# Kernel tuning notes

Measured on AMD Instinct MI355X. Metric: run time of the kernel, lower is better.

## Reference

```python
import jax, jax.numpy as jnp
import numpy as np

B, S, E = 4, 4096, 128  # batch, seq_len, embedding_dim (quaternion groups)
D = 4 * E               # flattened feature dim fed to the Linear layers


def setup_inputs() -> dict:
    key = jax.random.key(0)
    ks = jax.random.split(key, 9)
    scale_w = 1.0 / np.sqrt(D).astype(np.float32)
    return {
        "query": jax.random.normal(ks[0], (B, S, E, 4), dtype=jnp.float32),
        "key": jax.random.normal(ks[1], (B, S, E, 4), dtype=jnp.float32),
        "value": jax.random.normal(ks[2], (B, S, E, 4), dtype=jnp.float32),
        "Wq": jax.random.normal(ks[3], (D, D), dtype=jnp.float32) * scale_w,
        "bq": jax.random.normal(ks[4], (D,), dtype=jnp.float32) * 0.01,
        "Wk": jax.random.normal(ks[5], (D, D), dtype=jnp.float32) * scale_w,
        "bk": jax.random.normal(ks[6], (D,), dtype=jnp.float32) * 0.01,
        "Wv": jax.random.normal(ks[7], (D, D), dtype=jnp.float32) * scale_w,
        "bv": jax.random.normal(ks[8], (D,), dtype=jnp.float32) * 0.01,
    }


def reference(query, key, value, Wq, bq, Wk, bk, Wv, bv):
    b, s = query.shape[0], query.shape[1]
    e = query.shape[2]  # embedding_dim
    # flatten quaternion dim: [B,S,E,4] -> [B,S,4E]
    q = query.reshape(b, s, -1)
    k = key.reshape(b, key.shape[1], -1)
    v = value.reshape(b, value.shape[1], -1)
    # torch nn.Linear: x @ W^T + bias
    Q = (q @ Wq.T + bq).reshape(b, s, -1, 4)
    K = (k @ Wk.T + bk).reshape(b, key.shape[1], -1, 4)
    V = (v @ Wv.T + bv).reshape(b, value.shape[1], -1, 4)
    # full QK^T over quaternion-grouped dims: [B,S,S]
    scores = jnp.einsum('bseq,bkeq->bsk', Q, K) / jnp.sqrt(jnp.float32(e))
    weights = jax.nn.softmax(scores, axis=-1)
    # faithful to the source: weights are summed over k and scale V at position s
    output = jnp.einsum('bsk,bseq->bseq', weights, V)
    return output, weights
```

## Files before the change

### kernel.cpp

```cpp
#include <hip/hip_runtime.h>
#include <cstdint>

typedef _Float16 h1;
typedef _Float16 h4 __attribute__((ext_vector_type(4)));
typedef _Float16 h8 __attribute__((ext_vector_type(8)));
typedef float    f4 __attribute__((ext_vector_type(4)));
typedef float    f32x4 __attribute__((ext_vector_type(4)));

#define NB 4
#define SL 4096
#define DD 512
#define MM (NB*SL)
#define SHIFT 12.0f

__global__ __launch_bounds__(256) void convert_all(
    const float* __restrict__ Xq, const float* __restrict__ Xk, const float* __restrict__ Xv,
    const float* __restrict__ Wq, const float* __restrict__ Wk, const float* __restrict__ Wv,
    h1* __restrict__ Xh, h1* __restrict__ Wh)
{
    const int xper = MM*DD/4;
    const int wper = DD*DD/4;
    const int xtot = 3*xper;
    int i = blockIdx.x * 256 + threadIdx.x;
    const float* src;
    h1* dst;
    int j;
    if (i < xtot) {
        int mat = i / xper; j = i - mat*xper;
        src = (mat==0) ? Xq : (mat==1 ? Xk : Xv);
        dst = Xh + (size_t)mat*MM*DD;
    } else {
        int t = i - xtot;
        if (t >= 3*wper) return;
        int mat = t / wper; j = t - mat*wper;
        src = (mat==0) ? Wq : (mat==1 ? Wk : Wv);
        dst = Wh + (size_t)mat*DD*DD;
    }
    f4 v = ((const f4*)src)[j];
    h4 hv;
    hv[0]=(h1)v[0]; hv[1]=(h1)v[1]; hv[2]=(h1)v[2]; hv[3]=(h1)v[3];
    ((h4*)dst)[j] = hv;
}

__device__ __forceinline__ void stage_tile(const h1* __restrict__ gbase,
                                           h1* lds, int w, int l)
{
    #pragma unroll
    for (int j = 0; j < 4; j++) {
        const int cc  = w*4 + j;
        const int row = cc*8 + (l >> 3);
        const int sc  = (l & 7) ^ (l >> 3);
        const h1* src = gbase + (size_t)row * DD + sc*8;
        void* dst = (char*)lds + cc*1024;
        __builtin_amdgcn_global_load_lds(
            (const __attribute__((address_space(1))) uint32_t*)src,
            (__attribute__((address_space(3))) uint32_t*)dst, 16, 0, 0);
    }
}

__device__ __forceinline__ void stage_half(const h1* __restrict__ gbase,
                                           char* ldsbase, int w, int l)
{
    #pragma unroll
    for (int j = 0; j < 2; j++) {
        const int cc  = w*2 + j;
        const int row = cc*8 + (l >> 3);
        const int sc  = (l & 7) ^ (l >> 3);
        const h1* src = gbase + (size_t)row * DD + sc*8;
        __builtin_amdgcn_global_load_lds(
            (const __attribute__((address_space(1))) uint32_t*)src,
            (__attribute__((address_space(3))) uint32_t*)(ldsbase + cc*1024), 16, 0, 0);
    }
}

__device__ __forceinline__ h8 lds_frag(const h1* lds, int row, int lc)
{
    const int chunk = lc ^ (row & 7);
    return *(const h8*)(lds + row*64 + chunk*8);
}

__global__ __launch_bounds__(256) void proj_gemm(
    const h1* __restrict__ Xh, const h1* __restrict__ Wh,
    const float* __restrict__ bq, const float* __restrict__ bk, const float* __restrict__ bv,
    h1* __restrict__ Qh, h1* __restrict__ Kh, float* __restrict__ Vout)
{
    const int prj = blockIdx.z;
    const h1* __restrict__ X    = Xh + (size_t)prj * MM * DD;
    const h1* __restrict__ W    = Wh + (size_t)prj * DD * DD;
    const float* __restrict__ bias = (prj==0) ? bq : (prj==1 ? bk : bv);

    const int m0 = blockIdx.y * 128;
    const int n0 = blockIdx.x * 128;

    __shared__ h1 As[128*64];
    __shared__ h1 Bs[128*64];

    const int tid  = threadIdx.x;
    const int lane = tid & 63;
    const int wid  = tid >> 6;
    const int wm = wid >> 1, wn = wid & 1;
    const int g  = lane >> 4, c = lane & 15;

    f32x4 acc[4][4];
    #pragma unroll
    for (int i = 0; i < 4; i++)
        #pragma unroll
        for (int j = 0; j < 4; j++) acc[i][j] = (f32x4){0.f, 0.f, 0.f, 0.f};

    for (int k0 = 0; k0 < DD; k0 += 64) {
        __syncthreads();
        stage_tile(X + (size_t)m0 * DD + k0, As, wid, lane);
        stage_tile(W + (size_t)n0 * DD + k0, Bs, wid, lane);
        __syncthreads();
        #pragma unroll
        for (int kk = 0; kk < 2; kk++) {
            h8 af[4], bf[4];
            #pragma unroll
            for (int mf = 0; mf < 4; mf++) af[mf] = lds_frag(As, wm*64 + mf*16 + c, kk*4 + g);
            #pragma unroll
            for (int nf = 0; nf < 4; nf++) bf[nf] = lds_frag(Bs, wn*64 + nf*16 + c, kk*4 + g);
            #pragma unroll
            for (int mf = 0; mf < 4; mf++)
                #pragma unroll
                for (int nf = 0; nf < 4; nf++)
                    acc[mf][nf] = __builtin_amdgcn_mfma_f32_16x16x32_f16(af[mf], bf[nf], acc[mf][nf], 0, 0, 0);
        }
    }

    float bv4[4];
    #pragma unroll
    for (int nf = 0; nf < 4; nf++) bv4[nf] = bias[n0 + wn*64 + nf*16 + c];

    #pragma unroll
    for (int mf = 0; mf < 4; mf++) {
        #pragma unroll
        for (int i = 0; i < 4; i++) {
            const int row = m0 + wm*64 + mf*16 + g*4 + i;
            #pragma unroll
            for (int nf = 0; nf < 4; nf++) {
                const int col = n0 + wn*64 + nf*16 + c;
                float vv = acc[mf][nf][i] + bv4[nf];
                if (prj == 0)      Qh[(size_t)row*DD + col] = (h1)vv;
                else if (prj == 1) Kh[(size_t)row*DD + col] = (h1)vv;
                else               Vout[(size_t)row*DD + col] = vv;
            }
        }
    }
}

__global__ __launch_bounds__(512) void scores_gemm_8ph(
    const h1* __restrict__ Qh, const h1* __restrict__ Kh,
    h1* __restrict__ Eh,
    float* __restrict__ partial)
{
    const int orig = blockIdx.x;
    const int swz  = (orig & 7) * 128 + (orig >> 3);
    const int b  = swz >> 8;
    const int t_ = swz & 255;
    const int ty = t_ >> 4;
    const int tx = t_ & 15;
    const int m0 = ty * 256;
    const int n0 = tx * 256;
    const h1* __restrict__ Qb = Qh + (size_t)b * SL * DD;
    const h1* __restrict__ Kb = Kh + (size_t)b * SL * DD;

    __shared__ h1 Albuf[2*256*64];
    __shared__ h1 Blbuf[2*256*64];
    const int SLOT_H = 256*64;
    const int SLOT_B = SLOT_H*2;

    const int tid  = threadIdx.x;
    const int lane = tid & 63;
    const int wid  = tid >> 6;
    const int wm = wid >> 2;
    const int wn = wid & 3;
    const int g  = lane >> 4, c = lane & 15;

    f32x4 acc[8][4];
    #pragma unroll
    for (int i = 0; i < 8; i++)
        #pragma unroll
        for (int j = 0; j < 4; j++) acc[i][j] = (f32x4){0.f, 0.f, 0.f, 0.f};

    stage_half(Qb + (size_t)m0*DD,            (char*)Albuf,          wid, lane);
    stage_half(Qb + (size_t)(m0+128)*DD,      (char*)Albuf + 16384,  wid, lane);
    stage_half(Kb + (size_t)n0*DD,            (char*)Blbuf,          wid, lane);
    stage_half(Kb + (size_t)(n0+128)*DD,      (char*)Blbuf + 16384,  wid, lane);
    asm volatile("s_waitcnt vmcnt(0)" ::: "memory");
    __builtin_amdgcn_s_barrier();

    for (int kt = 0; kt < 8; ++kt) {
        const int cur = kt & 1;
        const h1* Abase = Albuf + cur*SLOT_H;
        const h1* Bbase = Blbuf + cur*SLOT_H;
        #pragma unroll
        for (int q = 0; q < 4; q++) {
            const int mh = q >> 1, nh = q & 1;

            h8 af[4][2], bf[2][2];
            #pragma unroll
            for (int fm = 0; fm < 4; fm++)
                #pragma unroll
                for (int ks = 0; ks < 2; ks++)
                    af[fm][ks] = lds_frag(Abase, wm*128 + (mh*4+fm)*16 + c, ks*4 + g);
            #pragma unroll
            for (int fn = 0; fn < 2; fn++)
                #pragma unroll
                for (int ks = 0; ks < 2; ks++)
                    bf[fn][ks] = lds_frag(Bbase, wn*64 + (nh*2+fn)*16 + c, ks*4 + g);

            if (q == 0 && kt < 7) {
                const int k0n = (kt+1) * 64;
                char* Adst = (char*)Albuf + (cur^1)*SLOT_B;
                char* Bdst = (char*)Blbuf + (cur^1)*SLOT_B;
                stage_half(Qb + (size_t)m0*DD + k0n,       Adst,         wid, lane);
                stage_half(Qb + (size_t)(m0+128)*DD + k0n, Adst + 16384, wid, lane);
                stage_half(Kb + (size_t)n0*DD + k0n,       Bdst,         wid, lane);
                stage_half(Kb + (size_t)(n0+128)*DD + k0n, Bdst + 16384, wid, lane);
            }

            __builtin_amdgcn_s_barrier();
            asm volatile("s_waitcnt lgkmcnt(0)" ::: "memory");
            __builtin_amdgcn_sched_barrier(0);
            __builtin_amdgcn_s_setprio(1);
            #pragma unroll
            for (int fm = 0; fm < 4; fm++)
                #pragma unroll
                for (int fn = 0; fn < 2; fn++)
                    #pragma unroll
                    for (int ks = 0; ks < 2; ks++)
                        acc[mh*4+fm][nh*2+fn] = __builtin_amdgcn_mfma_f32_16x16x32_f16(
                            af[fm][ks], bf[fn][ks], acc[mh*4+fm][nh*2+fn], 0, 0, 0);
            __builtin_amdgcn_s_setprio(0);
            if (q == 3) asm volatile("s_waitcnt vmcnt(0)" ::: "memory");
            __builtin_amdgcn_s_barrier();
        }
    }

    const float inv_scale = 0.08838834764831845f;
    #pragma unroll
    for (int mf = 0; mf < 8; mf++) {
        #pragma unroll
        for (int i = 0; i < 4; i++) {
            const int row = m0 + wm*128 + mf*16 + g*4 + i;
            h1* erow = Eh + ((size_t)b * SL + row) * SL;
            float rsum = 0.f;
            #pragma unroll
            for (int nf = 0; nf < 4; nf++) {
                const int col = n0 + wn*64 + nf*16 + c;
                float e = __expf(fmaf(acc[mf][nf][i], inv_scale, -SHIFT));
                erow[col] = (h1)e;
                rsum += e;
            }
            #pragma unroll
            for (int off = 1; off < 16; off <<= 1) rsum += __shfl_xor(rsum, off);
            if (c == 0)
                partial[((size_t)b * SL + row) * 64 + tx * 4 + wn] = rsum;
        }
    }
}

__global__ __launch_bounds__(256) void rowsum_inv(
    const float* __restrict__ partial, float* __restrict__ invrow)
{
    int row = blockIdx.x * 256 + threadIdx.x;
    const f4* p = (const f4*)(partial + (size_t)row * 64);
    float s = 0.f;
    #pragma unroll
    for (int i = 0; i < 16; i++) { f4 v = p[i]; s += v[0] + v[1] + v[2] + v[3]; }
    invrow[row] = 1.0f / s;
}

__global__ __launch_bounds__(256) void normalize_k(
    const h1* __restrict__ Eh, const float* __restrict__ invrow,
    float* __restrict__ Wout)
{
    const size_t total8 = (size_t)NB * SL * SL / 8;
    size_t i = (size_t)blockIdx.x * blockDim.x + threadIdx.x;
    const size_t stride = (size_t)gridDim.x * blockDim.x;
    for (; i < total8; i += stride) {
        const int row = (int)(i >> 9);
        h8 v = ((const h8*)Eh)[i];
        const float s = invrow[row];
        f4 o0, o1;
        #pragma unroll
        for (int j = 0; j < 4; j++) { o0[j] = (float)v[j] * s; o1[j] = (float)v[4+j] * s; }
        ((f4*)Wout)[i*2]   = o0;
        ((f4*)Wout)[i*2+1] = o1;
    }
}

extern "C" void kernel_launch(void* const* d_in, const int* in_sizes, int n_in,
                              void* d_out, int out_size, void* d_ws, size_t ws_size,
                              hipStream_t stream)
{
    const float* q  = (const float*)d_in[0];
    const float* k  = (const float*)d_in[1];
    const float* v  = (const float*)d_in[2];
    const float* Wq = (const float*)d_in[3];
    const float* bq = (const float*)d_in[4];
    const float* Wk = (const float*)d_in[5];
    const float* bk = (const float*)d_in[6];
    const float* Wv = (const float*)d_in[7];
    const float* bv = (const float*)d_in[8];

    float* out  = (float*)d_out;
    float* Vout = out;
    float* Wout = out + (size_t)MM * DD;

    char* ws = (char*)d_ws;
    h1* Xh = (h1*)ws;
    h1* Wh = (h1*)(ws + (size_t)3*MM*DD*2);
    h1* Qh = (h1*)((char*)Wh + (size_t)3*DD*DD*2);
    h1* Kh = (h1*)((char*)Qh + (size_t)MM*DD*2);
    float* partial = (float*)((char*)Kh + (size_t)MM*DD*2);
    float* invrow  = (float*)((char*)partial + (size_t)MM*64*4);
    h1* Eh = (h1*)((char*)invrow + (size_t)MM*4);

    const int conv_chunks = (3*MM*DD + 3*DD*DD) / 4;
    convert_all<<<(conv_chunks + 255)/256, 256, 0, stream>>>(q, k, v, Wq, Wk, Wv, Xh, Wh);
    proj_gemm<<<dim3(4, 128, 3), 256, 0, stream>>>(Xh, Wh, bq, bk, bv, Qh, Kh, Vout);
    scores_gemm_8ph<<<1024, 512, 0, stream>>>(Qh, Kh, Eh, partial);
    rowsum_inv<<<MM / 256, 256, 0, stream>>>(partial, invrow);
    normalize_k<<<2048, 256, 0, stream>>>(Eh, invrow, Wout);
}
```

Baseline: 286.5 us.

## Restructure scores GEMM into 4-slot, 3-deep K32 prefetch pipeline

Replaces the double-buffered K=64 staging with a four-slot ring of K=32 tiles prefetched three steps ahead. Each step runs two MFMA phases (top and bottom halves of M) that reuse the B fragments, and uses fractional vmcnt waits so that several tile loads stay in flight. It also switches to a new 32-wide LDS layout with an XOR swizzle. The aim is to hide global-load latency better. In exchange there are twice as many K iterations with more barriers per step, and the LDS footprint stays the same.

```diff
diff --git a/kernel.cpp b/kernel.cpp
--- a/kernel.cpp
+++ b/kernel.cpp
@@ -58,21 +58,6 @@
     }
 }
 
-__device__ __forceinline__ void stage_half(const h1* __restrict__ gbase,
-                                           char* ldsbase, int w, int l)
-{
-    #pragma unroll
-    for (int j = 0; j < 2; j++) {
-        const int cc  = w*2 + j;
-        const int row = cc*8 + (l >> 3);
-        const int sc  = (l & 7) ^ (l >> 3);
-        const h1* src = gbase + (size_t)row * DD + sc*8;
-        __builtin_amdgcn_global_load_lds(
-            (const __attribute__((address_space(1))) uint32_t*)src,
-            (__attribute__((address_space(3))) uint32_t*)(ldsbase + cc*1024), 16, 0, 0);
-    }
-}
-
 __device__ __forceinline__ h8 lds_frag(const h1* lds, int row, int lc)
 {
     const int chunk = lc ^ (row & 7);
@@ -146,6 +131,29 @@
             }
         }
     }
+}
+
+__device__ __forceinline__ void stage_slot32(const h1* __restrict__ gbase,
+                                             char* ldsbase, int w, int l)
+{
+    #pragma unroll
+    for (int j = 0; j < 2; j++) {
+        const int lc  = j*512 + w*64 + l;
+        const int row = lc >> 2;
+        const int ch  = lc & 3;
+        const int sc  = ch ^ ((row >> 1) & 3);
+        const h1* src = gbase + (size_t)row * DD + sc*8;
+        __builtin_amdgcn_global_load_lds(
+            (const __attribute__((address_space(1))) uint32_t*)src,
+            (__attribute__((address_space(3))) uint32_t*)(ldsbase + (size_t)(j*512 + w*64)*16),
+            16, 0, 0);
+    }
+}
+
+__device__ __forceinline__ h8 frag32(const h1* lds, int row, int g)
+{
+    const int ch = g ^ ((row >> 1) & 3);
+    return *(const h8*)(lds + row*32 + ch*8);
 }
 
 __global__ __launch_bounds__(512) void scores_gemm_8ph(
@@ -164,9 +172,9 @@
     const h1* __restrict__ Qb = Qh + (size_t)b * SL * DD;
     const h1* __restrict__ Kb = Kh + (size_t)b * SL * DD;
 
-    __shared__ h1 Albuf[2*256*64];
-    __shared__ h1 Blbuf[2*256*64];
-    const int SLOT_H = 256*64;
+    __shared__ h1 Albuf[4*256*32];
+    __shared__ h1 Blbuf[4*256*32];
+    const int SLOT_H = 256*32;
     const int SLOT_B = SLOT_H*2;
 
     const int tid  = threadIdx.x;
@@ -182,59 +190,61 @@
         #pragma unroll
         for (int j = 0; j < 4; j++) acc[i][j] = (f32x4){0.f, 0.f, 0.f, 0.f};
 
-    stage_half(Qb + (size_t)m0*DD,            (char*)Albuf,          wid, lane);
-    stage_half(Qb + (size_t)(m0+128)*DD,      (char*)Albuf + 16384,  wid, lane);
-    stage_half(Kb + (size_t)n0*DD,            (char*)Blbuf,          wid, lane);
-    stage_half(Kb + (size_t)(n0+128)*DD,      (char*)Blbuf + 16384,  wid, lane);
-    asm volatile("s_waitcnt vmcnt(0)" ::: "memory");
+    #pragma unroll
+    for (int kt = 0; kt < 3; ++kt) {
+        stage_slot32(Qb + (size_t)m0*DD + kt*32, (char*)Albuf + kt*SLOT_B, wid, lane);
+        stage_slot32(Kb + (size_t)n0*DD + kt*32, (char*)Blbuf + kt*SLOT_B, wid, lane);
+    }
+    asm volatile("s_waitcnt vmcnt(8)" ::: "memory");
     __builtin_amdgcn_s_barrier();
 
-    for (int kt = 0; kt < 8; ++kt) {
-        const int cur = kt & 1;
+    for (int kt = 0; kt < 16; ++kt) {
+        const int cur = kt & 3;
         const h1* Abase = Albuf + cur*SLOT_H;
         const h1* Bbase = Blbuf + cur*SLOT_H;
-        #pragma unroll
-        for (int q = 0; q < 4; q++) {
-            const int mh = q >> 1, nh = q & 1;
-
-            h8 af[4][2], bf[2][2];
-            #pragma unroll
-            for (int fm = 0; fm < 4; fm++)
-                #pragma unroll
-                for (int ks = 0; ks < 2; ks++)
-                    af[fm][ks] = lds_frag(Abase, wm*128 + (mh*4+fm)*16 + c, ks*4 + g);
-            #pragma unroll
-            for (int fn = 0; fn < 2; fn++)
-                #pragma unroll
-                for (int ks = 0; ks < 2; ks++)
-                    bf[fn][ks] = lds_frag(Bbase, wn*64 + (nh*2+fn)*16 + c, ks*4 + g);
-
-            if (q == 0 && kt < 7) {
-                const int k0n = (kt+1) * 64;
-                char* Adst = (char*)Albuf + (cur^1)*SLOT_B;
-                char* Bdst = (char*)Blbuf + (cur^1)*SLOT_B;
-                stage_half(Qb + (size_t)m0*DD + k0n,       Adst,         wid, lane);
-                stage_half(Qb + (size_t)(m0+128)*DD + k0n, Adst + 16384, wid, lane);
-                stage_half(Kb + (size_t)n0*DD + k0n,       Bdst,         wid, lane);
-                stage_half(Kb + (size_t)(n0+128)*DD + k0n, Bdst + 16384, wid, lane);
-            }
-
-            __builtin_amdgcn_s_barrier();
-            asm volatile("s_waitcnt lgkmcnt(0)" ::: "memory");
-            __builtin_amdgcn_sched_barrier(0);
-            __builtin_amdgcn_s_setprio(1);
-            #pragma unroll
-            for (int fm = 0; fm < 4; fm++)
-                #pragma unroll
-                for (int fn = 0; fn < 2; fn++)
-                    #pragma unroll
-                    for (int ks = 0; ks < 2; ks++)
-                        acc[mh*4+fm][nh*2+fn] = __builtin_amdgcn_mfma_f32_16x16x32_f16(
-                            af[fm][ks], bf[fn][ks], acc[mh*4+fm][nh*2+fn], 0, 0, 0);
-            __builtin_amdgcn_s_setprio(0);
-            if (q == 3) asm volatile("s_waitcnt vmcnt(0)" ::: "memory");
-            __builtin_amdgcn_s_barrier();
+
+        h8 af[4], bf[4];
+        #pragma unroll
+        for (int fm = 0; fm < 4; fm++) af[fm] = frag32(Abase, wm*128 + fm*16 + c, g);
+        #pragma unroll
+        for (int fn = 0; fn < 4; fn++) bf[fn] = frag32(Bbase, wn*64 + fn*16 + c, g);
+
+        if (kt <= 12) {
+            const int nk = kt + 3, ns = nk & 3;
+            stage_slot32(Qb + (size_t)m0*DD + nk*32, (char*)Albuf + ns*SLOT_B, wid, lane);
+            stage_slot32(Kb + (size_t)n0*DD + nk*32, (char*)Blbuf + ns*SLOT_B, wid, lane);
         }
+
+        __builtin_amdgcn_s_barrier();
+        asm volatile("s_waitcnt lgkmcnt(0)" ::: "memory");
+        __builtin_amdgcn_sched_barrier(0);
+        __builtin_amdgcn_s_setprio(1);
+        #pragma unroll
+        for (int fm = 0; fm < 4; fm++)
+            #pragma unroll
+            for (int fn = 0; fn < 4; fn++)
+                acc[fm][fn] = __builtin_amdgcn_mfma_f32_16x16x32_f16(af[fm], bf[fn], acc[fm][fn], 0, 0, 0);
+        __builtin_amdgcn_s_setprio(0);
+        __builtin_amdgcn_s_barrier();
+
+        #pragma unroll
+        for (int fm = 0; fm < 4; fm++) af[fm] = frag32(Abase, wm*128 + 64 + fm*16 + c, g);
+
+        __builtin_amdgcn_s_barrier();
+        asm volatile("s_waitcnt lgkmcnt(0)" ::: "memory");
+        __builtin_amdgcn_sched_barrier(0);
+        __builtin_amdgcn_s_setprio(1);
+        #pragma unroll
+        for (int fm = 0; fm < 4; fm++)
+            #pragma unroll
+            for (int fn = 0; fn < 4; fn++)
+                acc[4+fm][fn] = __builtin_amdgcn_mfma_f32_16x16x32_f16(af[fm], bf[fn], acc[4+fm][fn], 0, 0, 0);
+        __builtin_amdgcn_s_setprio(0);
+
+        if (kt <= 12)      { asm volatile("s_waitcnt vmcnt(8)" ::: "memory"); }
+        else if (kt == 13) { asm volatile("s_waitcnt vmcnt(4)" ::: "memory"); }
+        else if (kt == 14) { asm volatile("s_waitcnt vmcnt(0)" ::: "memory"); }
+        __builtin_amdgcn_s_barrier();
     }
 
     const float inv_scale = 0.08838834764831845f;
```

Measured after the change: 285.3 us. Within noise of the previous version (-0.4%).
